# Performance work log

Measured on AMD Instinct MI355X. Metric: run time of the kernel, lower is better.

The kernel has to match this reference:

```python
import jax, jax.numpy as jnp
import numpy as np

N_NODES = 100000
N_EDGES = 1600000
D = 64
NUM_HOPS = 3


def setup_inputs() -> dict:
    key = jax.random.key(0)
    ks = jax.random.split(key, 8)
    return {
        "H_l": jax.random.normal(ks[0], (N_NODES, D), dtype=jnp.float32),
        "edge_row": jax.random.randint(ks[1], (N_EDGES,), 0, N_NODES, dtype=jnp.int64),
        "edge_col": jax.random.randint(ks[2], (N_EDGES,), 0, N_NODES, dtype=jnp.int64),
        "edge_val": jax.random.uniform(ks[3], (N_EDGES,), dtype=jnp.float32),
        "out_degree": jax.random.uniform(ks[4], (N_NODES,), dtype=jnp.float32),
        "in_degree": jax.random.uniform(ks[5], (N_NODES,), dtype=jnp.float32),
        "hop_attention": jnp.ones((NUM_HOPS,), dtype=jnp.float32),
        "theta_out": jnp.full((NUM_HOPS,), 0.5, dtype=jnp.float32),
        "theta_in": jnp.full((NUM_HOPS,), 0.5, dtype=jnp.float32),
        "Theta": jax.random.normal(ks[6], (D, D), dtype=jnp.float32) * (6.0 ** 0.5) / (2 * D) ** 0.5,
    }


def reference(H_l, edge_row, edge_col, edge_val, out_degree, in_degree,
              hop_attention, theta_out, theta_in, Theta):
    n = H_l.shape[0]
    num_hops = hop_attention.shape[0]
    alpha = jax.nn.softmax(hop_attention)

    def spmm(rows, cols, X):
        # (A @ X)[r] = sum over edges (r,c): val * X[c]
        return jax.ops.segment_sum(edge_val[:, None] * X[cols], rows, num_segments=n)

    # fixed degree-scaled features (degrees clamped as in __init__)
    X_out = jnp.maximum(out_degree, 1e-8)[:, None] * H_l
    X_in = jnp.maximum(in_degree, 1e-8)[:, None] * H_l
    sum_term = jnp.zeros_like(H_l)
    for k in range(num_hops):
        # A^{k+1} @ (D_out H) computed by one more application of A per hop
        X_out = spmm(edge_row, edge_col, X_out)
        # (A^{k+1})^T @ (D_in H): transpose swaps row/col roles
        X_in = spmm(edge_col, edge_row, X_in)
        sum_term = sum_term + alpha[k] * (theta_out[k] * X_out + theta_in[k] * X_in)

    conv_term = jax.nn.sigmoid(sum_term @ Theta)
    return conv_term + H_l
```

## Files before the change

### kernel.cpp

```cpp
#include <hip/hip_runtime.h>
#include <hip/hip_fp16.h>

#define DFEAT 64
#define BKT_SHIFT 8
#define BKT_NODES 256
#define NBMAX 512
#define CH 4096
#define SRC_BITS 17
#define SRC_MASK ((1 << SRC_BITS) - 1)

__device__ __forceinline__ unsigned short f2h(float f) {
    return __half_as_ushort(__float2half(f));
}
__device__ __forceinline__ float h2f(unsigned short u) {
    return __half2float(__ushort_as_half(u));
}

__global__ void init_kernel(const float* __restrict__ H,
                            const float* __restrict__ outdeg,
                            const float* __restrict__ indeg,
                            const float* __restrict__ hop_att,
                            const float* __restrict__ th_out,
                            const float* __restrict__ th_in,
                            unsigned short* __restrict__ XAout,
                            unsigned short* __restrict__ XAin,
                            float* __restrict__ coefs, int n4) {
    int idx = blockIdx.x * blockDim.x + threadIdx.x;
    if (idx == 0) {
        float m = fmaxf(fmaxf(hop_att[0], hop_att[1]), hop_att[2]);
        float e0 = __expf(hop_att[0] - m);
        float e1 = __expf(hop_att[1] - m);
        float e2 = __expf(hop_att[2] - m);
        float inv = 1.0f / (e0 + e1 + e2);
        coefs[0] = e0 * inv * th_out[0]; coefs[1] = e0 * inv * th_in[0];
        coefs[2] = e1 * inv * th_out[1]; coefs[3] = e1 * inv * th_in[1];
        coefs[4] = e2 * inv * th_out[2]; coefs[5] = e2 * inv * th_in[2];
    }
    if (idx >= n4) return;
    int row = idx >> 4;
    float4 h = reinterpret_cast<const float4*>(H)[idx];
    float doo = fmaxf(outdeg[row], 1e-8f);
    float dii = fmaxf(indeg[row], 1e-8f);
    reinterpret_cast<ushort4*>(XAout)[idx] =
        make_ushort4(f2h(h.x * doo), f2h(h.y * doo), f2h(h.z * doo), f2h(h.w * doo));
    reinterpret_cast<ushort4*>(XAin)[idx] =
        make_ushort4(f2h(h.x * dii), f2h(h.y * dii), f2h(h.z * dii), f2h(h.w * dii));
}

__global__ __launch_bounds__(256) void hist2d_kernel(
        const int* __restrict__ erow, const int* __restrict__ ecol,
        int* __restrict__ cnt2, int nEdges, int nB, int nBlkA) {
    __shared__ int hR[NBMAX], hC[NBMAX];
    int k = blockIdx.x;
    for (int i = threadIdx.x; i < nB; i += 256) { hR[i] = 0; hC[i] = 0; }
    __syncthreads();
    int base = k * CH;
    int nV = min(CH, nEdges - base);
    for (int i = threadIdx.x; i < nV; i += 256) {
        atomicAdd(&hR[erow[base + i] >> BKT_SHIFT], 1);
        atomicAdd(&hC[ecol[base + i] >> BKT_SHIFT], 1);
    }
    __syncthreads();
    for (int b = threadIdx.x; b < nB; b += 256) {
        cnt2[(size_t)b * nBlkA + k] = hR[b];
        cnt2[((size_t)nB + b) * nBlkA + k] = hC[b];
    }
}

__global__ void scan_reduce1(const int* __restrict__ p, int* __restrict__ bsum,
                             int n) {
    int t = threadIdx.x, lane = t & 63, wid = t >> 6;
    int base = blockIdx.x * 1024 + t * 4;
    int s = 0;
#pragma unroll
    for (int i = 0; i < 4; ++i) { int idx = base + i; if (idx < n) s += p[idx]; }
#pragma unroll
    for (int o = 32; o >= 1; o >>= 1) s += __shfl_down(s, o, 64);
    __shared__ int wsum[4];
    if (lane == 0) wsum[wid] = s;
    __syncthreads();
    if (t == 0) bsum[blockIdx.x] = wsum[0] + wsum[1] + wsum[2] + wsum[3];
}

__global__ void scan_spine1(int* __restrict__ bsum, int nChunks) {
    int lane = threadIdx.x;
    int carry = 0;
    for (int base = 0; base < nChunks; base += 64) {
        int i = base + lane;
        int v = (i < nChunks) ? bsum[i] : 0;
        int s = v;
#pragma unroll
        for (int o = 1; o < 64; o <<= 1) {
            int x = __shfl_up(s, o, 64);
            if (lane >= o) s += x;
        }
        if (i < nChunks) bsum[i] = carry + s - v;
        carry += __shfl(s, 63, 64);
    }
}

__global__ void scan_down1(int* __restrict__ p, const int* __restrict__ bsum,
                           int n) {
    int t = threadIdx.x, lane = t & 63, wid = t >> 6;
    int base = blockIdx.x * 1024 + t * 4;
    int v[4];
    int tsum = 0;
#pragma unroll
    for (int i = 0; i < 4; ++i) {
        v[i] = (base + i < n) ? p[base + i] : 0;
        tsum += v[i];
    }
    int inc = tsum;
#pragma unroll
    for (int o = 1; o < 64; o <<= 1) {
        int x = __shfl_up(inc, o, 64);
        if (lane >= o) inc += x;
    }
    __shared__ int wsum[4];
    if (lane == 63) wsum[wid] = inc;
    __syncthreads();
    int woff = 0;
    for (int w = 0; w < wid; ++w) woff += wsum[w];
    int run = bsum[blockIdx.x] + woff + inc - tsum;
#pragma unroll
    for (int i = 0; i < 4; ++i) {
        if (base + i < n) p[base + i] = run;
        run += v[i];
    }
}

__global__ __launch_bounds__(256) void partA_kernel(
        const int* __restrict__ erow, const int* __restrict__ ecol,
        const float* __restrict__ eval, const int* __restrict__ base2,
        unsigned* __restrict__ recRkey, unsigned short* __restrict__ recRval,
        unsigned* __restrict__ recCkey, unsigned short* __restrict__ recCval,
        int nEdges, int nB, int nBlkA) {
    __shared__ int hist[NBMAX], scn[NBMAX], cur[NBMAX], gbase[NBMAX];
    __shared__ unsigned short keybuf[CH], slotKey[CH];
    __shared__ unsigned stageK[CH];
    __shared__ unsigned short stageV[CH];
    int dir = blockIdx.y;
    const int* dk = dir ? ecol : erow;
    const int* ds = dir ? erow : ecol;
    unsigned* recK = dir ? recCkey : recRkey;
    unsigned short* recV = dir ? recCval : recRval;
    int k = blockIdx.x;
    int base = k * CH;
    int nV = min(CH, nEdges - base);
    for (int i = threadIdx.x; i < nB; i += 256) {
        hist[i] = 0; cur[i] = 0;
        gbase[i] = base2[((size_t)dir * nB + i) * nBlkA + k] - dir * nEdges;
    }
    __syncthreads();
    for (int i = threadIdx.x; i < nV; i += 256) {
        int key = dk[base + i] >> BKT_SHIFT;
        keybuf[i] = (unsigned short)key;
        atomicAdd(&hist[key], 1);
    }
    __syncthreads();
    if (threadIdx.x < 64) {
        int lane = threadIdx.x;
        int carry = 0;
        for (int bb = 0; bb < nB; bb += 64) {
            int i = bb + lane;
            int v = (i < nB) ? hist[i] : 0;
            int s = v;
#pragma unroll
            for (int o = 1; o < 64; o <<= 1) {
                int x = __shfl_up(s, o, 64);
                if (lane >= o) s += x;
            }
            if (i < nB) scn[i] = carry + s - v;
            carry += __shfl(s, 63, 64);
        }
    }
    __syncthreads();
    for (int i = threadIdx.x; i < nV; i += 256) {
        int e = base + i;
        int key = keybuf[i];
        int slot = scn[key] + atomicAdd(&cur[key], 1);
        int dl = dk[e] & (BKT_NODES - 1);
        stageK[slot] = (unsigned)ds[e] | ((unsigned)dl << SRC_BITS);
        stageV[slot] = f2h(eval[e]);
        slotKey[slot] = (unsigned short)key;
    }
    __syncthreads();
    for (int i = threadIdx.x; i < nV; i += 256) {
        int key = slotKey[i];
        int o = gbase[key] + (i - scn[key]);
        recK[o] = stageK[i];
        recV[o] = stageV[i];
    }
}

__global__ __launch_bounds__(256) void partB_kernel(
        const unsigned* __restrict__ recRkey, const unsigned short* __restrict__ recRval,
        const unsigned* __restrict__ recCkey, const unsigned short* __restrict__ recCval,
        const int* __restrict__ base2,
        int* __restrict__ rowptr, int* __restrict__ colptr,
        unsigned* __restrict__ pairsR, unsigned* __restrict__ pairsC,
        int nEdges, int nB, int nBlkA, int nNodes) {
    __shared__ int hist[BKT_NODES], scn[BKT_NODES], cur[BKT_NODES];
    int dir = blockIdx.y;
    int b = blockIdx.x;
    const unsigned* recK = dir ? recCkey : recRkey;
    const unsigned short* recV = dir ? recCval : recRval;
    unsigned* pairs = dir ? pairsC : pairsR;
    int* nptr = dir ? colptr : rowptr;
    int segB = base2[((size_t)dir * nB + b) * nBlkA] - dir * nEdges;
    int segE = (b == nB - 1) ? nEdges
             : base2[((size_t)dir * nB + b + 1) * nBlkA] - dir * nEdges;
    int t = threadIdx.x;
    hist[t] = 0; cur[t] = 0;
    __syncthreads();
    for (int j = segB + t; j < segE; j += 256)
        atomicAdd(&hist[(recK[j] >> SRC_BITS) & (BKT_NODES - 1)], 1);
    __syncthreads();
    if (t < 64) {
        int lane = t, carry = 0;
        for (int bb = 0; bb < BKT_NODES; bb += 64) {
            int i = bb + lane;
            int v = hist[i], s = v;
#pragma unroll
            for (int o = 1; o < 64; o <<= 1) {
                int x = __shfl_up(s, o, 64);
                if (lane >= o) s += x;
            }
            scn[i] = carry + s - v;
            carry += __shfl(s, 63, 64);
        }
    }
    __syncthreads();
    int node = (b << BKT_SHIFT) + t;
    if (node < nNodes) nptr[node] = segB + scn[t];
    if (b == nB - 1 && t == 0) nptr[nNodes] = nEdges;
    for (int j = segB + t; j < segE; j += 256) {
        unsigned key = recK[j];
        int dl = (key >> SRC_BITS) & (BKT_NODES - 1);
        int slot = segB + scn[dl] + atomicAdd(&cur[dl], 1);
        pairs[slot] = ((key & SRC_MASK) << 15) | (recV[j] & 0x7FFFu);
    }
}

__device__ __forceinline__ void gather_rows(
        const int* __restrict__ ptr, const unsigned* __restrict__ pairs,
        const __half* __restrict__ X, int node, int hb, int sub,
        float& axo, float& ayo) {
    float2 a0{0.f,0.f}, a1{0.f,0.f}, a2{0.f,0.f}, a3{0.f,0.f};
    float2 a4{0.f,0.f}, a5{0.f,0.f}, a6{0.f,0.f}, a7{0.f,0.f};
    int j = ptr[node], eE = ptr[node + 1];
    auto step = [&](int jj, float2& a) {
        unsigned p = pairs[jj + hb];
        float2 x = __half22float2(*(const __half2*)(X + (p >> 15) * DFEAT + 2 * sub));
        float v = h2f(p & 0x7FFFu);
        a.x += v * x.x; a.y += v * x.y;
    };
    for (; j + 16 <= eE; j += 16) {
        step(j, a0);      step(j + 2, a1);  step(j + 4, a2);  step(j + 6, a3);
        step(j + 8, a4);  step(j + 10, a5); step(j + 12, a6); step(j + 14, a7);
    }
    if (j + 8 <= eE) {
        step(j, a0); step(j + 2, a1); step(j + 4, a2); step(j + 6, a3);
        j += 8;
    }
#pragma unroll
    for (int q = 0; q < 4; ++q) {
        int idx = j + 2 * q + hb;
        unsigned p = (idx < eE) ? pairs[idx] : 0u;
        float2 x = __half22float2(*(const __half2*)(X + (p >> 15) * DFEAT + 2 * sub));
        float v = h2f(p & 0x7FFFu);
        a4.x += v * x.x; a4.y += v * x.y;
    }
    float ax = ((a0.x + a1.x) + (a2.x + a3.x)) + ((a4.x + a5.x) + (a6.x + a7.x));
    float ay = ((a0.y + a1.y) + (a2.y + a3.y)) + ((a4.y + a5.y) + (a6.y + a7.y));
    ax += __shfl_xor(ax, 32, 64);
    ay += __shfl_xor(ay, 32, 64);
    axo = ax; ayo = ay;
}

template <int FIRST, int WRITEY>
__global__ __launch_bounds__(256) void spmm_split(
        const int* __restrict__ rowptr, const unsigned* __restrict__ pairsR,
        const int* __restrict__ colptr, const unsigned* __restrict__ pairsC,
        const __half* __restrict__ Xout, const __half* __restrict__ Xin,
        unsigned short* __restrict__ Yout, unsigned short* __restrict__ Yin,
        unsigned short* __restrict__ sumO, unsigned short* __restrict__ sumI,
        const float* __restrict__ coefs, int k, int nNodes) {
    int b = blockIdx.x;
    int slot = b & 7;
    int dir = slot >> 2;
    int g = (b >> 3) * 4 + (slot & 3);
    int wid = threadIdx.x >> 6;
    int lane = threadIdx.x & 63;
    int node = g * 4 + wid;
    if (node >= nNodes) return;

    const int* ptr = dir ? colptr : rowptr;
    const unsigned* pairs = dir ? pairsC : pairsR;
    const __half* X = dir ? Xin : Xout;
    unsigned short* Y = dir ? Yin : Yout;
    unsigned short* sm = dir ? sumI : sumO;
    float cf = coefs[2 * k + dir];

    int hb = lane >> 5;
    int sub = lane & 31;

    float ax, ay;
    gather_rows(ptr, pairs, X, node, hb, sub, ax, ay);

    if (hb == 0) {
        int off = node * DFEAT + 2 * sub;
        if (WRITEY) {
            __half2 yv = __floats2half2_rn(ax, ay);
            __builtin_nontemporal_store(*reinterpret_cast<unsigned*>(&yv),
                                        reinterpret_cast<unsigned*>(Y + off));
        }
        float sx = cf * ax, sy = cf * ay;
        if (!FIRST) {
            __half2 old = *reinterpret_cast<const __half2*>(sm + off);
            float2 of = __half22float2(old);
            sx += of.x; sy += of.y;
        }
        __half2 sv = __floats2half2_rn(sx, sy);
        __builtin_nontemporal_store(*reinterpret_cast<unsigned*>(&sv),
                                    reinterpret_cast<unsigned*>(sm + off));
    }
}

__global__ __launch_bounds__(256) void final_kernel(
        const unsigned short* __restrict__ sumO,
        const unsigned short* __restrict__ sumI,
        const float* __restrict__ H, const float* __restrict__ Theta,
        float* __restrict__ out, int nRows) {
    __shared__ float Th[64 * 64];
    __shared__ float S[32 * 64];
    int t = threadIdx.x;
    for (int i = t; i < 64 * 64; i += 256) Th[i] = Theta[i];
    int rbase = blockIdx.x * 32;
    for (int i = t; i < 32 * 64; i += 256) {
        int r = rbase + (i >> 6);
        float v = 0.f;
        if (r < nRows) {
            int off = r * DFEAT + (i & 63);
            v = h2f(sumO[off]) + h2f(sumI[off]);
        }
        S[i] = v;
    }
    __syncthreads();
    int c = t & 63;
#pragma unroll
    for (int rr = 0; rr < 8; ++rr) {
        int rl = (t >> 6) + rr * 4;
        int row = rbase + rl;
        float acc = 0.f;
#pragma unroll
        for (int kk = 0; kk < 64; ++kk)
            acc += S[rl * 64 + kk] * Th[kk * 64 + c];
        if (row < nRows) {
            float r = 1.0f / (1.0f + __expf(-acc)) + H[row * DFEAT + c];
            __builtin_nontemporal_store(r, &out[row * DFEAT + c]);
        }
    }
}

extern "C" void kernel_launch(void* const* d_in, const int* in_sizes, int n_in,
                              void* d_out, int out_size, void* d_ws, size_t ws_size,
                              hipStream_t stream) {
    const float* H      = (const float*)d_in[0];
    const int*   erow   = (const int*)d_in[1];
    const int*   ecol   = (const int*)d_in[2];
    const float* eval   = (const float*)d_in[3];
    const float* outdeg = (const float*)d_in[4];
    const float* indeg  = (const float*)d_in[5];
    const float* hopatt = (const float*)d_in[6];
    const float* thout  = (const float*)d_in[7];
    const float* thin   = (const float*)d_in[8];
    const float* Theta  = (const float*)d_in[9];
    float* out = (float*)d_out;

    int nNodes = in_sizes[0] / DFEAT;
    int nEdges = in_sizes[1];

    char* ws = (char*)d_ws;
    size_t off = 0;
    auto alloc = [&](size_t bytes) {
        void* p = ws + off;
        off += (bytes + 255) & ~(size_t)255;
        return p;
    };
    size_t xBytes = (size_t)nNodes * DFEAT * sizeof(unsigned short);
    unsigned short* XAout = (unsigned short*)alloc(xBytes);
    unsigned short* XAin  = (unsigned short*)alloc(xBytes);
    unsigned short* XBout = (unsigned short*)alloc(xBytes);
    unsigned short* XBin  = (unsigned short*)alloc(xBytes);
    unsigned short* sumO  = (unsigned short*)alloc(xBytes);
    unsigned short* sumI  = (unsigned short*)alloc(xBytes);
    int*   rowptr = (int*)alloc((size_t)(nNodes + 1) * sizeof(int));
    int*   colptr = (int*)alloc((size_t)(nNodes + 1) * sizeof(int));
    unsigned*       recRkey = (unsigned*)alloc((size_t)nEdges * sizeof(unsigned));
    unsigned short* recRval = (unsigned short*)alloc((size_t)nEdges * sizeof(unsigned short));
    unsigned*       recCkey = (unsigned*)alloc((size_t)nEdges * sizeof(unsigned));
    unsigned short* recCval = (unsigned short*)alloc((size_t)nEdges * sizeof(unsigned short));
    unsigned* pairsR = (unsigned*)alloc((size_t)nEdges * sizeof(unsigned));
    unsigned* pairsC = (unsigned*)alloc((size_t)nEdges * sizeof(unsigned));

    int nB    = (nNodes + BKT_NODES - 1) >> BKT_SHIFT;
    int nBlkA = (nEdges + CH - 1) / CH;
    int L = 2 * nB * nBlkA;
    int nChunks = (L + 1023) / 1024;
    int*   cnt2 = (int*)alloc((size_t)L * sizeof(int));
    int*   bsum = (int*)alloc((size_t)nChunks * sizeof(int));
    float* coefs = (float*)alloc(8 * sizeof(float));

    int n4 = nNodes * (DFEAT / 4);
    int ewBlocks = (n4 + 255) / 256;
    int gPerDir = (nNodes + 3) / 4;
    int grid8 = (gPerDir + 3) / 4;
    int splitGrid = 8 * grid8;

    init_kernel<<<ewBlocks, 256, 0, stream>>>(H, outdeg, indeg, hopatt, thout, thin,
                                              XAout, XAin, coefs, n4);
    hist2d_kernel<<<nBlkA, 256, 0, stream>>>(erow, ecol, cnt2, nEdges, nB, nBlkA);
    scan_reduce1<<<nChunks, 256, 0, stream>>>(cnt2, bsum, L);
    scan_spine1<<<1, 64, 0, stream>>>(bsum, nChunks);
    scan_down1<<<nChunks, 256, 0, stream>>>(cnt2, bsum, L);
    partA_kernel<<<dim3(nBlkA, 2), 256, 0, stream>>>(erow, ecol, eval, cnt2,
                                                     recRkey, recRval, recCkey, recCval,
                                                     nEdges, nB, nBlkA);
    partB_kernel<<<dim3(nB, 2), 256, 0, stream>>>(recRkey, recRval, recCkey, recCval,
                                                  cnt2, rowptr, colptr, pairsR, pairsC,
                                                  nEdges, nB, nBlkA, nNodes);

    spmm_split<1, 1><<<splitGrid, 256, 0, stream>>>(rowptr, pairsR, colptr, pairsC,
                                                    (const __half*)XAout, (const __half*)XAin,
                                                    XBout, XBin, sumO, sumI,
                                                    coefs, 0, nNodes);
    spmm_split<0, 1><<<splitGrid, 256, 0, stream>>>(rowptr, pairsR, colptr, pairsC,
                                                    (const __half*)XBout, (const __half*)XBin,
                                                    XAout, XAin, sumO, sumI,
                                                    coefs, 1, nNodes);
    spmm_split<0, 0><<<splitGrid, 256, 0, stream>>>(rowptr, pairsR, colptr, pairsC,
                                                    (const __half*)XAout, (const __half*)XAin,
                                                    nullptr, nullptr, sumO, sumI,
                                                    coefs, 2, nNodes);

    final_kernel<<<(nNodes + 31) / 32, 256, 0, stream>>>(sumO, sumI, H, Theta,
                                                         out, nNodes);
}
```

Baseline: 433.8 us.

## Split feature matrices into four 16-column slabs for cache-local SpMM gathers

Feature arrays are re-laid out as four quarter slabs of 16 half-precision columns each, stored node-major within a slab. Each SpMM block handles one slab and one direction, and a wave processes 8 edges at once with 8 lanes per edge. The goal is for each slab (about 3.2 MB per direction) to fit better in cache, so random row gathers hit more often. The cost is that every edge's pair list is now read four times, once per slab, plus an extra shuffle reduction. The pair loads also become nontemporal.

After: 884.9 us. 2.04x slower.

```diff
diff --git a/kernel.cpp b/kernel.cpp
--- a/kernel.cpp
+++ b/kernel.cpp
@@ -2,6 +2,7 @@
 #include <hip/hip_fp16.h>
 
 #define DFEAT 64
+#define QDIM 16
 #define BKT_SHIFT 8
 #define BKT_NODES 256
 #define NBMAX 512
@@ -24,7 +25,7 @@
                             const float* __restrict__ th_in,
                             unsigned short* __restrict__ XAout,
                             unsigned short* __restrict__ XAin,
-                            float* __restrict__ coefs, int n4) {
+                            float* __restrict__ coefs, int n4, int nNodes) {
     int idx = blockIdx.x * blockDim.x + threadIdx.x;
     if (idx == 0) {
         float m = fmaxf(fmaxf(hop_att[0], hop_att[1]), hop_att[2]);
@@ -37,13 +38,17 @@
         coefs[4] = e2 * inv * th_out[2]; coefs[5] = e2 * inv * th_in[2];
     }
     if (idx >= n4) return;
-    int row = idx >> 4;
+    int node = idx >> 4;
+    int dg = idx & 15;
+    int q = dg >> 2;
+    int o = (dg & 3) * 4;
     float4 h = reinterpret_cast<const float4*>(H)[idx];
-    float doo = fmaxf(outdeg[row], 1e-8f);
-    float dii = fmaxf(indeg[row], 1e-8f);
-    reinterpret_cast<ushort4*>(XAout)[idx] =
+    float doo = fmaxf(outdeg[node], 1e-8f);
+    float dii = fmaxf(indeg[node], 1e-8f);
+    size_t qoff = ((size_t)q * nNodes + node) * QDIM + o;
+    *reinterpret_cast<ushort4*>(XAout + qoff) =
         make_ushort4(f2h(h.x * doo), f2h(h.y * doo), f2h(h.z * doo), f2h(h.w * doo));
-    reinterpret_cast<ushort4*>(XAin)[idx] =
+    *reinterpret_cast<ushort4*>(XAin + qoff) =
         make_ushort4(f2h(h.x * dii), f2h(h.y * dii), f2h(h.z * dii), f2h(h.w * dii));
 }
 
@@ -242,44 +247,8 @@
     }
 }
 
-__device__ __forceinline__ void gather_rows(
-        const int* __restrict__ ptr, const unsigned* __restrict__ pairs,
-        const __half* __restrict__ X, int node, int hb, int sub,
-        float& axo, float& ayo) {
-    float2 a0{0.f,0.f}, a1{0.f,0.f}, a2{0.f,0.f}, a3{0.f,0.f};
-    float2 a4{0.f,0.f}, a5{0.f,0.f}, a6{0.f,0.f}, a7{0.f,0.f};
-    int j = ptr[node], eE = ptr[node + 1];
-    auto step = [&](int jj, float2& a) {
-        unsigned p = pairs[jj + hb];
-        float2 x = __half22float2(*(const __half2*)(X + (p >> 15) * DFEAT + 2 * sub));
-        float v = h2f(p & 0x7FFFu);
-        a.x += v * x.x; a.y += v * x.y;
-    };
-    for (; j + 16 <= eE; j += 16) {
-        step(j, a0);      step(j + 2, a1);  step(j + 4, a2);  step(j + 6, a3);
-        step(j + 8, a4);  step(j + 10, a5); step(j + 12, a6); step(j + 14, a7);
-    }
-    if (j + 8 <= eE) {
-        step(j, a0); step(j + 2, a1); step(j + 4, a2); step(j + 6, a3);
-        j += 8;
-    }
-#pragma unroll
-    for (int q = 0; q < 4; ++q) {
-        int idx = j + 2 * q + hb;
-        unsigned p = (idx < eE) ? pairs[idx] : 0u;
-        float2 x = __half22float2(*(const __half2*)(X + (p >> 15) * DFEAT + 2 * sub));
-        float v = h2f(p & 0x7FFFu);
-        a4.x += v * x.x; a4.y += v * x.y;
-    }
-    float ax = ((a0.x + a1.x) + (a2.x + a3.x)) + ((a4.x + a5.x) + (a6.x + a7.x));
-    float ay = ((a0.y + a1.y) + (a2.y + a3.y)) + ((a4.y + a5.y) + (a6.y + a7.y));
-    ax += __shfl_xor(ax, 32, 64);
-    ay += __shfl_xor(ay, 32, 64);
-    axo = ax; ayo = ay;
-}
-
 template <int FIRST, int WRITEY>
-__global__ __launch_bounds__(256) void spmm_split(
+__global__ __launch_bounds__(256) void spmm_q(
         const int* __restrict__ rowptr, const unsigned* __restrict__ pairsR,
         const int* __restrict__ colptr, const unsigned* __restrict__ pairsC,
         const __half* __restrict__ Xout, const __half* __restrict__ Xin,
@@ -289,7 +258,8 @@
     int b = blockIdx.x;
     int slot = b & 7;
     int dir = slot >> 2;
-    int g = (b >> 3) * 4 + (slot & 3);
+    int q = slot & 3;
+    int g = b >> 3;
     int wid = threadIdx.x >> 6;
     int lane = threadIdx.x & 63;
     int node = g * 4 + wid;
@@ -297,19 +267,44 @@
 
     const int* ptr = dir ? colptr : rowptr;
     const unsigned* pairs = dir ? pairsC : pairsR;
-    const __half* X = dir ? Xin : Xout;
-    unsigned short* Y = dir ? Yin : Yout;
-    unsigned short* sm = dir ? sumI : sumO;
+    size_t qbase = (size_t)q * nNodes * QDIM;
+    const __half* X = (dir ? Xin : Xout) + qbase;
+    unsigned short* Y = (dir ? Yin : Yout);
+    unsigned short* sm = (dir ? sumI : sumO);
     float cf = coefs[2 * k + dir];
 
-    int hb = lane >> 5;
-    int sub = lane & 31;
-
-    float ax, ay;
-    gather_rows(ptr, pairs, X, node, hb, sub, ax, ay);
-
-    if (hb == 0) {
-        int off = node * DFEAT + 2 * sub;
+    int se = lane >> 3;
+    int dp = lane & 7;
+
+    float ax0 = 0.f, ay0 = 0.f, ax1 = 0.f, ay1 = 0.f;
+    int j = ptr[node], eE = ptr[node + 1];
+    for (; j + 16 <= eE; j += 16) {
+        unsigned p0 = __builtin_nontemporal_load(&pairs[j + se]);
+        unsigned p1 = __builtin_nontemporal_load(&pairs[j + 8 + se]);
+        float2 x0 = __half22float2(*(const __half2*)(X + (p0 >> 15) * QDIM + 2 * dp));
+        float2 x1 = __half22float2(*(const __half2*)(X + (p1 >> 15) * QDIM + 2 * dp));
+        float v0 = h2f(p0 & 0x7FFFu);
+        float v1 = h2f(p1 & 0x7FFFu);
+        ax0 += v0 * x0.x; ay0 += v0 * x0.y;
+        ax1 += v1 * x1.x; ay1 += v1 * x1.y;
+    }
+    for (; j < eE; j += 8) {
+        int idx = j + se;
+        unsigned p = (idx < eE) ? __builtin_nontemporal_load(&pairs[idx]) : 0u;
+        float2 x = __half22float2(*(const __half2*)(X + (p >> 15) * QDIM + 2 * dp));
+        float v = h2f(p & 0x7FFFu);
+        ax0 += v * x.x; ay0 += v * x.y;
+    }
+    float ax = ax0 + ax1, ay = ay0 + ay1;
+    ax += __shfl_xor(ax, 8, 64);
+    ay += __shfl_xor(ay, 8, 64);
+    ax += __shfl_xor(ax, 16, 64);
+    ay += __shfl_xor(ay, 16, 64);
+    ax += __shfl_xor(ax, 32, 64);
+    ay += __shfl_xor(ay, 32, 64);
+
+    if (se == 0) {
+        size_t off = qbase + (size_t)node * QDIM + 2 * dp;
         if (WRITEY) {
             __half2 yv = __floats2half2_rn(ax, ay);
             __builtin_nontemporal_store(*reinterpret_cast<unsigned*>(&yv),
@@ -339,9 +334,10 @@
     int rbase = blockIdx.x * 32;
     for (int i = t; i < 32 * 64; i += 256) {
         int r = rbase + (i >> 6);
+        int c = i & 63;
         float v = 0.f;
         if (r < nRows) {
-            int off = r * DFEAT + (i & 63);
+            size_t off = ((size_t)(c >> 4) * nRows + r) * QDIM + (c & 15);
             v = h2f(sumO[off]) + h2f(sumI[off]);
         }
         S[i] = v;
@@ -414,12 +410,10 @@
 
     int n4 = nNodes * (DFEAT / 4);
     int ewBlocks = (n4 + 255) / 256;
-    int gPerDir = (nNodes + 3) / 4;
-    int grid8 = (gPerDir + 3) / 4;
-    int splitGrid = 8 * grid8;
+    int qGrid = 8 * ((nNodes + 3) / 4);
 
     init_kernel<<<ewBlocks, 256, 0, stream>>>(H, outdeg, indeg, hopatt, thout, thin,
-                                              XAout, XAin, coefs, n4);
+                                              XAout, XAin, coefs, n4, nNodes);
     hist2d_kernel<<<nBlkA, 256, 0, stream>>>(erow, ecol, cnt2, nEdges, nB, nBlkA);
     scan_reduce1<<<nChunks, 256, 0, stream>>>(cnt2, bsum, L);
     scan_spine1<<<1, 64, 0, stream>>>(bsum, nChunks);
@@ -431,18 +425,18 @@
                                                   cnt2, rowptr, colptr, pairsR, pairsC,
                                                   nEdges, nB, nBlkA, nNodes);
 
-    spmm_split<1, 1><<<splitGrid, 256, 0, stream>>>(rowptr, pairsR, colptr, pairsC,
-                                                    (const __half*)XAout, (const __half*)XAin,
-                                                    XBout, XBin, sumO, sumI,
-                                                    coefs, 0, nNodes);
-    spmm_split<0, 1><<<splitGrid, 256, 0, stream>>>(rowptr, pairsR, colptr, pairsC,
-                                                    (const __half*)XBout, (const __half*)XBin,
-                                                    XAout, XAin, sumO, sumI,
-                                                    coefs, 1, nNodes);
-    spmm_split<0, 0><<<splitGrid, 256, 0, stream>>>(rowptr, pairsR, colptr, pairsC,
-                                                    (const __half*)XAout, (const __half*)XAin,
-                                                    nullptr, nullptr, sumO, sumI,
-                                                    coefs, 2, nNodes);
+    spmm_q<1, 1><<<qGrid, 256, 0, stream>>>(rowptr, pairsR, colptr, pairsC,
+                                            (const __half*)XAout, (const __half*)XAin,
+                                            XBout, XBin, sumO, sumI,
+                                            coefs, 0, nNodes);
+    spmm_q<0, 1><<<qGrid, 256, 0, stream>>>(rowptr, pairsR, colptr, pairsC,
+                                            (const __half*)XBout, (const __half*)XBin,
+                                            XAout, XAin, sumO, sumI,
+                                            coefs, 1, nNodes);
+    spmm_q<0, 0><<<qGrid, 256, 0, stream>>>(rowptr, pairsR, colptr, pairsC,
+                                            (const __half*)XAout, (const __half*)XAin,
+                                            nullptr, nullptr, sumO, sumI,
+                                            coefs, 2, nNodes);
 
     final_kernel<<<(nNodes + 31) / 32, 256, 0, stream>>>(sumO, sumI, H, Theta,
                                                          out, nNodes);
```
